# Kernel optimization log

Measured on AMD Instinct MI355X. Metric: run time of the kernel, lower is better.

## Reference

```python
import jax, jax.numpy as jnp
import numpy as np

EPS = 1e-5

def _bn(x, g, b):
    # training-mode batchnorm over all axes except the last (channel)
    axes = tuple(range(x.ndim - 1))
    m = x.mean(axis=axes, keepdims=True)
    v = x.var(axis=axes, keepdims=True)
    return (x - m) * jax.lax.rsqrt(v + EPS) * g + b

def setup_inputs() -> dict:
    key = jax.random.key(0)
    ks = jax.random.split(key, 9)
    B, N = 4, 4096
    def w(i, shape, fan_in):
        return jax.random.normal(ks[i], shape, jnp.float32) * np.float32(1.0 / np.sqrt(fan_in))
    return {
        "x": jax.random.normal(ks[0], (B, 3, N), jnp.float32),
        "Wq": w(1, (64, 3), 3),
        "Wkv": w(2, (128, 3), 3),
        "Wp1": w(3, (64, 3), 3),
        "Wp2": w(4, (64, 64), 64),
        "Wa": w(5, (64, 64), 64),
        "Wc1": w(6, (64, 64), 64),
        "Wsk": w(7, (64, 6), 6),
        "Wga": w(8, (64, 128), 128),
        "g_p": jnp.ones(64, jnp.float32), "b_p": jnp.zeros(64, jnp.float32),
        "g_a": jnp.ones(64, jnp.float32), "b_a": jnp.zeros(64, jnp.float32),
        "g_c": jnp.ones(64, jnp.float32), "b_c": jnp.zeros(64, jnp.float32),
        "g_sk": jnp.ones(64, jnp.float32), "b_sk": jnp.zeros(64, jnp.float32),
        "g_ga": jnp.ones(64, jnp.float32), "b_ga": jnp.zeros(64, jnp.float32),
        "k": 32,
    }

def reference(x, Wq, Wkv, Wp1, Wp2, Wa, Wc1, Wsk, Wga,
              g_p, b_p, g_a, b_a, g_c, b_c, g_sk, b_sk, g_ga, b_ga, k):
    # x: [B, 3, N] point cloud
    xt = jnp.transpose(x, (0, 2, 1))                      # [B, N, 3]
    B = xt.shape[0]
    # --- KNN neighbor grouping (irregular gather) ---
    sq = jnp.sum(xt * xt, axis=-1)                        # [B, N]
    dist = sq[:, :, None] + sq[:, None, :] - 2.0 * jnp.einsum('bnc,bmc->bnm', xt, xt)
    _, idx = jax.lax.top_k(-dist, k)                      # [B, N, k]
    grouped = xt[jnp.arange(B)[:, None, None], idx]       # [B, N, k, 3]
    rel = grouped - xt[:, :, None, :]                     # relative coords
    # --- local self-attention (1x1 conv QKV + position encoding) ---
    q = jnp.einsum('bnc,dc->bnd', xt, Wq)[:, :, None, :]  # [B, N, 1, 64]
    kv = jnp.einsum('bnkc,dc->bnkd', rel, Wkv)            # [B, N, k, 128]
    kf, vf = kv[..., :64], kv[..., 64:]
    pos = jnp.einsum('bnkd,ed->bnke',
                     jax.nn.relu(_bn(jnp.einsum('bnkc,dc->bnkd', rel, Wp1), g_p, b_p)),
                     Wp2)                                 # [B, N, k, 64]
    logits = jax.nn.relu(_bn(jnp.einsum('bnkd,ed->bnke', q - kf + pos, Wa), g_a, b_a))
    attn = jax.nn.softmax(logits, axis=2)                 # softmax over k neighbors
    agg = jnp.sum(attn * (vf + pos), axis=2)              # [B, N, 64]
    # --- pointnet conv-BN head + skip + fusion ---
    h = jax.nn.relu(_bn(jnp.einsum('bnd,ed->bne', agg, Wc1), g_c, b_c))
    nb_max = jnp.max(grouped, axis=2)                     # [B, N, 3] max-pool over neighbors
    sk = jax.nn.relu(_bn(jnp.einsum('bnc,dc->bnd',
                                    jnp.concatenate([xt, nb_max], axis=-1), Wsk), g_sk, b_sk))
    out = jax.nn.relu(_bn(jnp.einsum('bnc,dc->bnd',
                                     jnp.concatenate([h, sk], axis=-1), Wga), g_ga, b_ga))
    return jnp.transpose(out, (0, 2, 1))                  # [B, 64, N]
```

## Files before the change

### kernel.cpp

```cpp
#include <hip/hip_runtime.h>

#define NBATCH 4
#define NPTS   4096
#define NP     (NBATCH*NPTS)
#define KK     32
#define INF    __builtin_inff()

static const size_t OFF_PTS  = 0;
static const size_t OFF_IDX  = 65536;
static const size_t OFF_TSK  = 589824;
static const size_t OFF_TC   = 1638400;
static const size_t OFF_TGA  = 2686976;
static const size_t OFF_PREL = 3735552;
static const size_t OFF_PSK  = 3735568;
static const size_t OFF_PTA  = 3735696;
static const size_t OFF_PTC  = 3735824;
static const size_t OFF_PTGA = 3735952;
static const size_t OFF_AFF  = 3736080;

typedef __bf16 bf16x8  __attribute__((ext_vector_type(8)));
typedef float  floatx16 __attribute__((ext_vector_type(16)));
#define MFMA32(a,b,c) __builtin_amdgcn_mfma_f32_32x32x16_bf16(a, b, c, 0, 0, 0)

union F8 { bf16x8 v; unsigned short us[8]; uint4 q4; };

__device__ __forceinline__ unsigned short bfbits(float f) {
  unsigned u = __float_as_uint(f);
  return (unsigned short)((u + 0x7FFFu + ((u >> 16) & 1u)) >> 16);
}
__device__ __forceinline__ floatx16 zero16() {
  floatx16 v;
#pragma unroll
  for (int i = 0; i < 16; ++i) v[i] = 0.f;
  return v;
}
__device__ __forceinline__ float wsum(float v) {
#pragma unroll
  for (int o = 32; o; o >>= 1) v += __shfl_xor(v, o, 64);
  return v;
}
__device__ __forceinline__ int isum(int v) {
#pragma unroll
  for (int o = 32; o; o >>= 1) v += __shfl_xor(v, o);
  return v;
}

__global__ __launch_bounds__(256,1) void k_prep(const float* __restrict__ x, float4* __restrict__ pts,
                                                float* __restrict__ pta, float* __restrict__ ptc,
                                                float* __restrict__ ptga, float* __restrict__ prel9,
                                                float* __restrict__ psk128) {
  if (blockIdx.x == 0) {
    if (threadIdx.x < 128) {
      pta[threadIdx.x] = 0.f; ptc[threadIdx.x] = 0.f; ptga[threadIdx.x] = 0.f;
      psk128[threadIdx.x] = 0.f;
    }
    if (threadIdx.x < 16) prel9[threadIdx.x] = 0.f;
  }
  int g = blockIdx.x * 256 + threadIdx.x;
  int b = g / NPTS, n = g % NPTS;
  float vx = x[(b*3+0)*NPTS + n];
  float vy = x[(b*3+1)*NPTS + n];
  float vz = x[(b*3+2)*NPTS + n];
  pts[g] = make_float4(vx, vy, vz, vx*vx + vy*vy + vz*vz);
}

__global__ __launch_bounds__(256) void k_knn(const float4* __restrict__ pts, int* __restrict__ idx,
                                             const float* __restrict__ Wsk, float* __restrict__ tsk,
                                             float* __restrict__ prel9, float* __restrict__ psk128) {
  __shared__ __align__(16) float4 tile[1024];
  __shared__ int ocnt[4];
  __shared__ int lsel[128];
  __shared__ float rsum[9], psum[64], pss[64];
  const int tid  = threadIdx.x;
  const int w    = tid >> 6;
  const int lane = tid & 63;
  if (tid < 9)  rsum[tid] = 0.f;
  if (tid < 64) { psum[tid] = 0.f; pss[tid] = 0.f; }
  __syncthreads();
  const int n = blockIdx.x * 4 + w;
  const int batch = n >> 12;
  const float4* base = pts + batch * NPTS;
  const float4 me = pts[n];
  const float wk0 = Wsk[lane*6+0], wk1 = Wsk[lane*6+1], wk2 = Wsk[lane*6+2],
              wk3 = Wsk[lane*6+3], wk4 = Wsk[lane*6+4], wk5 = Wsk[lane*6+5];

  unsigned keys[64];
  unsigned t0 = 0xFFFFFFFFu, t1 = 0xFFFFFFFFu, t2 = 0xFFFFFFFFu, t3 = 0xFFFFFFFFu;
  for (int st = 0; st < 4; ++st) {
    __syncthreads();
#pragma unroll
    for (int r = 0; r < 4; ++r)
      tile[r*256 + tid] = base[st*1024 + r*256 + tid];
    __syncthreads();
#pragma unroll
    for (int j = 0; j < 16; ++j) {
      float4 p = tile[j*64 + lane];
      float dot = fmaf(me.x, p.x, fmaf(me.y, p.y, me.z * p.z));
      float d = fmaxf(fmaf(-2.f, dot, me.w + p.w), 0.f);
      unsigned k = __float_as_uint(d);
      keys[st*16 + j] = k;
      unsigned m = k, x;
      x = min(t0, m); m = max(t0, m); t0 = x;
      x = min(t1, m); m = max(t1, m); t1 = x;
      x = min(t2, m); m = max(t2, m); t2 = x;
      t3 = min(t3, m);
    }
  }

  unsigned glo = t0, ghi = t3;
#pragma unroll
  for (int o = 32; o; o >>= 1) {
    glo = min(glo, (unsigned)__shfl_xor((int)glo, o));
    ghi = max(ghi, (unsigned)__shfl_xor((int)ghi, o));
  }

  unsigned lo = glo, hi = ghi, tau = ghi;
  bool exact = false;
  while (lo < hi) {
    unsigned mid = lo + ((hi - lo) >> 1);
    int c = (t0 <= mid) + (t1 <= mid) + (t2 <= mid) + (t3 <= mid);
    c = isum(c);
    if (c == 32) { tau = mid; exact = true; break; }
    if (c > 32) hi = mid; else lo = mid + 1;
  }
  if (!exact) tau = lo;

  if (__ballot(t3 <= tau) != 0ull) {
    lo = glo; hi = tau; exact = false;
    while (lo < hi) {
      unsigned mid = lo + ((hi - lo) >> 1);
      int c = 0;
#pragma unroll
      for (int t = 0; t < 64; ++t) c += (keys[t] <= mid) ? 1 : 0;
      c = isum(c);
      if (c == 32) { tau = mid; exact = true; break; }
      if (c > 32) hi = mid; else lo = mid + 1;
    }
    if (!exact) tau = lo;
  }

  if (lane == 0) ocnt[w] = 0;
  int* op = idx + n * KK;
#pragma unroll
  for (int t = 0; t < 64; ++t) {
    bool take = exact ? (keys[t] <= tau) : (keys[t] < tau);
    if (take) {
      int s = atomicAdd(&ocnt[w], 1);
      int m = (t >> 4) * 1024 + (t & 15) * 64 + lane;
      op[s] = m; lsel[w*32 + s] = m;
    }
  }
  if (!exact) {
    unsigned long long em = 0;
#pragma unroll
    for (int t = 0; t < 64; ++t) if (keys[t] == tau) em |= 1ull << t;
    int n1 = ocnt[w];
    int need = 32 - n1;
    for (int f = 0; f < need; ++f) {
      int myt = em ? (int)__builtin_ctzll(em) : 64;
      int mym = (myt < 64) ? ((myt >> 4) * 1024 + (myt & 15) * 64 + lane) : 0x7FFFFFFF;
      int g = mym;
#pragma unroll
      for (int o = 32; o; o >>= 1) g = min(g, __shfl_xor(g, o));
      if (mym == g && myt < 64) { em &= em - 1; op[n1 + f] = mym; lsel[w*32 + n1 + f] = mym; }
    }
  }

  int mi = lsel[w*32 + (lane & 31)];
  float4 p = base[mi];
  bool act = lane < 32;
  float r0 = act ? p.x - me.x : 0.f;
  float r1 = act ? p.y - me.y : 0.f;
  float r2 = act ? p.z - me.z : 0.f;
  float vals[9] = { r0, r1, r2, r0*r0, r0*r1, r0*r2, r1*r1, r1*r2, r2*r2 };
#pragma unroll
  for (int t = 0; t < 9; ++t) {
    float rs = wsum(vals[t]);
    if (lane == 0) atomicAdd(&rsum[t], rs);
  }
  float nx = act ? p.x : -INF, ny = act ? p.y : -INF, nz = act ? p.z : -INF;
#pragma unroll
  for (int o = 32; o; o >>= 1) {
    nx = fmaxf(nx, __shfl_xor(nx, o));
    ny = fmaxf(ny, __shfl_xor(ny, o));
    nz = fmaxf(nz, __shfl_xor(nz, o));
  }
  float ts = fmaf(me.x, wk0, fmaf(me.y, wk1, fmaf(me.z, wk2,
             fmaf(nx, wk3, fmaf(ny, wk4, nz * wk5)))));
  tsk[n*64 + lane] = ts;
  atomicAdd(&psum[lane], ts);
  atomicAdd(&pss[lane], ts * ts);
  __syncthreads();
  if (tid < 9)  atomicAdd(&prel9[tid], rsum[tid]);
  if (tid < 64) atomicAdd(&psk128[tid], psum[tid]);
  else if (tid < 128) atomicAdd(&psk128[tid], pss[tid - 64]);
}

__global__ __launch_bounds__(64,1) void k_fin1(const float* __restrict__ prel9, const float* __restrict__ psk128,
                                               const float* __restrict__ Wp1,
                                               const float* __restrict__ g_p, const float* __restrict__ b_p,
                                               const float* __restrict__ g_sk, const float* __restrict__ b_sk,
                                               float* __restrict__ aff) {
  int d = threadIdx.x;
  double C = (double)NP * (double)KK;
  double mr0 = prel9[0]/C, mr1 = prel9[1]/C, mr2 = prel9[2]/C;
  double e00 = prel9[3]/C, e01 = prel9[4]/C, e02 = prel9[5]/C;
  double e11 = prel9[6]/C, e12 = prel9[7]/C, e22 = prel9[8]/C;
  double w0 = Wp1[d*3+0], w1 = Wp1[d*3+1], w2 = Wp1[d*3+2];
  double mu  = w0*mr0 + w1*mr1 + w2*mr2;
  double ex2 = w0*w0*e00 + w1*w1*e11 + w2*w2*e22 + 2.0*(w0*w1*e01 + w0*w2*e02 + w1*w2*e12);
  double var = ex2 - mu*mu;
  double sc  = (double)g_p[d] / sqrt(var + 1e-5);
  aff[0*64 + d] = (float)sc;
  aff[1*64 + d] = (float)((double)b_p[d] - mu*sc);
  double mean = (double)psk128[d] / (double)NP;
  double v2   = (double)psk128[64+d] / (double)NP - mean*mean;
  double sc4  = (double)g_sk[d] / sqrt(v2 + 1e-5);
  aff[6*64 + d] = (float)sc4;
  aff[7*64 + d] = (float)((double)b_sk[d] - mean*sc4);
}

__global__ __launch_bounds__(64,1) void k_fin2(const float* __restrict__ st, double C,
                                               const float* __restrict__ g, const float* __restrict__ b,
                                               float* __restrict__ s_out, float* __restrict__ o_out) {
  int d = threadIdx.x;
  double mean = (double)st[d] / C;
  double var  = (double)st[64 + d] / C - mean*mean;
  double sc   = (double)g[d] / sqrt(var + 1e-5);
  s_out[d] = (float)sc;
  o_out[d] = (float)((double)b[d] - mean*sc);
}

template<int MODE>
__global__ __launch_bounds__(256,1) void k_entry(const float4* __restrict__ pts, const int* __restrict__ idx,
                                                 const float* __restrict__ Wq, const float* __restrict__ Wkv,
                                                 const float* __restrict__ Wp1, const float* __restrict__ Wp2,
                                                 const float* __restrict__ Wa, const float* __restrict__ Wc1,
                                                 const float* __restrict__ aff, float* __restrict__ pstats,
                                                 float* __restrict__ tc) {
  __shared__ __align__(16) unsigned short ybuf[4][32][72];
  __shared__ __align__(16) float aggbuf[4][64];
  __shared__ float psum[64], pss[64];
  if (threadIdx.x < 64) { psum[threadIdx.x] = 0.f; pss[threadIdx.x] = 0.f; }
  __syncthreads();
  const int lane = threadIdx.x & 63;
  const int w    = threadIdx.x >> 6;
  const int c    = lane & 31;
  const int q5   = lane >> 5;

  F8 B0[2];
#pragma unroll
  for (int nt = 0; nt < 2; ++nt)
#pragma unroll
    for (int t = 0; t < 8; ++t)
      B0[nt].us[t] = (q5 == 0 && t < 3) ? bfbits(Wp1[(nt*32+c)*3 + t]) : (unsigned short)0;

  F8 Bs[4][2], B2[4][2];
#pragma unroll
  for (int kt = 0; kt < 4; ++kt)
#pragma unroll
    for (int h = 0; h < 2; ++h) {
      const float* p2 = Wp2 + (h*32+c)*64 + kt*16 + q5*8;
      float4 a = *(const float4*)p2, b = *(const float4*)(p2 + 4);
      Bs[kt][h].us[0]=bfbits(a.x); Bs[kt][h].us[1]=bfbits(a.y); Bs[kt][h].us[2]=bfbits(a.z); Bs[kt][h].us[3]=bfbits(a.w);
      Bs[kt][h].us[4]=bfbits(b.x); Bs[kt][h].us[5]=bfbits(b.y); Bs[kt][h].us[6]=bfbits(b.z); Bs[kt][h].us[7]=bfbits(b.w);
      const float* pa = Wa + (h*32+c)*64 + kt*16 + q5*8;
      float4 e = *(const float4*)pa, f = *(const float4*)(pa + 4);
      B2[kt][h].us[0]=bfbits(e.x); B2[kt][h].us[1]=bfbits(e.y); B2[kt][h].us[2]=bfbits(e.z); B2[kt][h].us[3]=bfbits(e.w);
      B2[kt][h].us[4]=bfbits(f.x); B2[kt][h].us[5]=bfbits(f.y); B2[kt][h].us[6]=bfbits(f.z); B2[kt][h].us[7]=bfbits(f.w);
    }

  F8 Bk4[4];
#pragma unroll
  for (int nt = 0; nt < 4; ++nt) {
    if (MODE == 0 && nt >= 2) { for (int t = 0; t < 8; ++t) Bk4[nt].us[t] = 0; continue; }
    int e = (nt & 1)*32 + c;
#pragma unroll
    for (int t = 0; t < 8; ++t)
      Bk4[nt].us[t] = (q5 == 0 && t < 3)
        ? bfbits(nt < 2 ? -Wkv[e*3 + t] : Wkv[(64+e)*3 + t]) : (unsigned short)0;
  }

  const float s1a = aff[c],      o1a = aff[64+c];
  const float s1b = aff[32+c],   o1b = aff[96+c];
  float s2a = 0.f, o2a = 0.f, s2b = 0.f, o2b = 0.f;
  if (MODE == 1) { s2a = aff[128+c]; o2a = aff[192+c]; s2b = aff[160+c]; o2b = aff[224+c]; }
  const float wqa0 = Wq[c*3+0],      wqa1 = Wq[c*3+1],      wqa2 = Wq[c*3+2];
  const float wqb0 = Wq[(32+c)*3+0], wqb1 = Wq[(32+c)*3+1], wqb2 = Wq[(32+c)*3+2];

  const int wave_id = blockIdx.x * 4 + w;
  const int n0 = wave_id * 8;
  const int batch = n0 >> 12;
  const float4* base = pts + batch * NPTS;

  float4 me = pts[n0];
  float4 pp = base[idx[n0*KK + c]];

  for (int pi = 0; pi < 8; ++pi) {
    const int n = n0 + pi;
    float4 men = me, ppn = pp;
    if (pi < 7) {
      men = pts[n + 1];
      ppn = base[idx[(n + 1)*KK + c]];
    }
    const float r0 = pp.x - me.x, r1 = pp.y - me.y, r2 = pp.z - me.z;
    F8 relA;
#pragma unroll
    for (int t = 0; t < 8; ++t) relA.us[t] = 0;
    if (q5 == 0) { relA.us[0] = bfbits(r0); relA.us[1] = bfbits(r1); relA.us[2] = bfbits(r2); }

    const floatx16 z = zero16();
    floatx16 y0 = MFMA32(relA.v, B0[0].v, z);
    floatx16 y1 = MFMA32(relA.v, B0[1].v, z);
#pragma unroll
    for (int r = 0; r < 16; ++r) {
      int row = (r & 3) + 8*(r >> 2) + 4*q5;
      ybuf[w][row][c]      = bfbits(fmaxf(fmaf(y0[r], s1a, o1a), 0.f));
      ybuf[w][row][32 + c] = bfbits(fmaxf(fmaf(y1[r], s1b, o1b), 0.f));
    }
    F8 Ay[4];
#pragma unroll
    for (int kt = 0; kt < 4; ++kt) Ay[kt].q4 = *(const uint4*)&ybuf[w][c][kt*16 + q5*8];

    floatx16 Cp0 = z, Cp1 = z;
#pragma unroll
    for (int kt = 0; kt < 4; ++kt) {
      Cp0 = MFMA32(Ay[kt].v, Bs[kt][0].v, Cp0);
      Cp1 = MFMA32(Ay[kt].v, Bs[kt][1].v, Cp1);
    }
    floatx16 Cu0 = MFMA32(relA.v, Bk4[0].v, Cp0);
    floatx16 Cu1 = MFMA32(relA.v, Bk4[1].v, Cp1);
    if (MODE == 1) {
      Cp0 = MFMA32(relA.v, Bk4[2].v, Cp0);
      Cp1 = MFMA32(relA.v, Bk4[3].v, Cp1);
    }
    const float qa = fmaf(me.x, wqa0, fmaf(me.y, wqa1, me.z * wqa2));
    const float qb = fmaf(me.x, wqb0, fmaf(me.y, wqb1, me.z * wqb2));
#pragma unroll
    for (int r = 0; r < 16; ++r) {
      int row = (r & 3) + 8*(r >> 2) + 4*q5;
      ybuf[w][row][c]      = bfbits(Cu0[r] + qa);
      ybuf[w][row][32 + c] = bfbits(Cu1[r] + qb);
    }
    F8 Au[4];
#pragma unroll
    for (int kt = 0; kt < 4; ++kt) Au[kt].q4 = *(const uint4*)&ybuf[w][c][kt*16 + q5*8];
    floatx16 Ct0 = z, Ct1 = z;
#pragma unroll
    for (int kt = 0; kt < 4; ++kt) {
      Ct0 = MFMA32(Au[kt].v, B2[kt][0].v, Ct0);
      Ct1 = MFMA32(Au[kt].v, B2[kt][1].v, Ct1);
    }

    if (MODE == 0) {
      float sa = 0.f, qqa = 0.f, sb = 0.f, qqb = 0.f;
#pragma unroll
      for (int r = 0; r < 16; ++r) {
        sa += Ct0[r]; qqa = fmaf(Ct0[r], Ct0[r], qqa);
        sb += Ct1[r]; qqb = fmaf(Ct1[r], Ct1[r], qqb);
      }
      sa += __shfl_xor(sa, 32); qqa += __shfl_xor(qqa, 32);
      sb += __shfl_xor(sb, 32); qqb += __shfl_xor(qqb, 32);
      if (q5 == 0) {
        atomicAdd(&psum[c], sa);      atomicAdd(&pss[c], qqa);
        atomicAdd(&psum[32+c], sb);   atomicAdd(&pss[32+c], qqb);
      }
    } else {
      float ma = -INF, mb = -INF;
#pragma unroll
      for (int r = 0; r < 16; ++r) {
        float la = fmaxf(fmaf(Ct0[r], s2a, o2a), 0.f); Ct0[r] = la; ma = fmaxf(ma, la);
        float lb = fmaxf(fmaf(Ct1[r], s2b, o2b), 0.f); Ct1[r] = lb; mb = fmaxf(mb, lb);
      }
      ma = fmaxf(ma, __shfl_xor(ma, 32));
      mb = fmaxf(mb, __shfl_xor(mb, 32));
      float sa = 0.f, sb = 0.f, aga = 0.f, agb = 0.f;
#pragma unroll
      for (int r = 0; r < 16; ++r) {
        float ta = __expf(Ct0[r] - ma); sa += ta; aga = fmaf(ta, Cp0[r], aga);
        float tb = __expf(Ct1[r] - mb); sb += tb; agb = fmaf(tb, Cp1[r], agb);
      }
      sa += __shfl_xor(sa, 32); aga += __shfl_xor(aga, 32);
      sb += __shfl_xor(sb, 32); agb += __shfl_xor(agb, 32);
      if (q5 == 0) {
        aggbuf[w][c]      = aga / sa;
        aggbuf[w][32 + c] = agb / sb;
      }
      float acc = 0.f;
#pragma unroll
      for (int g = 0; g < 16; ++g) {
        float4 av = *(const float4*)&aggbuf[w][g*4];
        const float4 wv = *(const float4*)(Wc1 + lane*64 + g*4);
        acc = fmaf(av.x, wv.x, fmaf(av.y, wv.y, fmaf(av.z, wv.z, fmaf(av.w, wv.w, acc))));
      }
      tc[n*64 + lane] = acc;
      atomicAdd(&psum[lane], acc);
      atomicAdd(&pss[lane], acc * acc);
    }
    me = men; pp = ppn;
  }
  __syncthreads();
  if (threadIdx.x < 64) atomicAdd(&pstats[threadIdx.x], psum[threadIdx.x]);
  else if (threadIdx.x < 128) atomicAdd(&pstats[threadIdx.x], pss[threadIdx.x - 64]);
}

__global__ __launch_bounds__(256,1) void k_final(const float* __restrict__ tcb, const float* __restrict__ tskb,
                                                 const float* __restrict__ Wga, const float* __restrict__ aff,
                                                 float* __restrict__ tga, float* __restrict__ pstats) {
  __shared__ __align__(16) float hb[4][64];
  __shared__ __align__(16) float sb[4][64];
  __shared__ float psum[64], pss[64];
  if (threadIdx.x < 64) { psum[threadIdx.x] = 0.f; pss[threadIdx.x] = 0.f; }
  __syncthreads();
  const int lane = threadIdx.x & 63;
  const int w    = threadIdx.x >> 6;
  const int n = blockIdx.x * 4 + w;
  hb[w][lane] = fmaxf(fmaf(tcb[n*64 + lane],  aff[256 + lane], aff[320 + lane]), 0.f);
  sb[w][lane] = fmaxf(fmaf(tskb[n*64 + lane], aff[384 + lane], aff[448 + lane]), 0.f);
  float g0=0,g1=0,g2=0,g3=0;
#pragma unroll
  for (int d = 0; d < 64; d += 4) {
    const float4 hv = *(const float4*)&hb[w][d];
    const float4 wg = *(const float4*)(Wga + lane*128 + d);
    g0 = fmaf(hv.x, wg.x, g0);
    g1 = fmaf(hv.y, wg.y, g1);
    g2 = fmaf(hv.z, wg.z, g2);
    g3 = fmaf(hv.w, wg.w, g3);
  }
#pragma unroll
  for (int d = 0; d < 64; d += 4) {
    const float4 sv = *(const float4*)&sb[w][d];
    const float4 wg = *(const float4*)(Wga + lane*128 + 64 + d);
    g0 = fmaf(sv.x, wg.x, g0);
    g1 = fmaf(sv.y, wg.y, g1);
    g2 = fmaf(sv.z, wg.z, g2);
    g3 = fmaf(sv.w, wg.w, g3);
  }
  const float tg = (g0+g1) + (g2+g3);
  tga[n*64 + lane] = tg;
  atomicAdd(&psum[lane], tg);
  atomicAdd(&pss[lane], tg * tg);
  __syncthreads();
  if (threadIdx.x < 64) atomicAdd(&pstats[threadIdx.x], psum[threadIdx.x]);
  else if (threadIdx.x < 128) atomicAdd(&pstats[threadIdx.x], pss[threadIdx.x - 64]);
}

__global__ __launch_bounds__(256,1) void k_out(const float* __restrict__ tga, const float* __restrict__ aff,
                                               float* __restrict__ out) {
  int g = blockIdx.x * 256 + threadIdx.x;
  int nn = g & 4095;
  int e  = (g >> 12) & 63;
  int b  = g >> 18;
  float v = tga[((b << 12) + nn) * 64 + e];
  out[g] = fmaxf(fmaf(v, aff[512 + e], aff[576 + e]), 0.f);
}

extern "C" void kernel_launch(void* const* d_in, const int* in_sizes, int n_in,
                              void* d_out, int out_size, void* d_ws, size_t ws_size,
                              hipStream_t stream) {
  const float* x    = (const float*)d_in[0];
  const float* Wq   = (const float*)d_in[1];
  const float* Wkv  = (const float*)d_in[2];
  const float* Wp1  = (const float*)d_in[3];
  const float* Wp2  = (const float*)d_in[4];
  const float* Wa   = (const float*)d_in[5];
  const float* Wc1  = (const float*)d_in[6];
  const float* Wsk  = (const float*)d_in[7];
  const float* Wga  = (const float*)d_in[8];
  const float* g_p  = (const float*)d_in[9];
  const float* b_p  = (const float*)d_in[10];
  const float* g_a  = (const float*)d_in[11];
  const float* b_a  = (const float*)d_in[12];
  const float* g_c  = (const float*)d_in[13];
  const float* b_c  = (const float*)d_in[14];
  const float* g_sk = (const float*)d_in[15];
  const float* b_sk = (const float*)d_in[16];
  const float* g_ga = (const float*)d_in[17];
  const float* b_ga = (const float*)d_in[18];
  float* W = (float*)d_ws;
  float4*  pts   = (float4*)(W + OFF_PTS);
  int*     idx   = (int*)(W + OFF_IDX);
  float*   tsk   = W + OFF_TSK;
  float*   tc    = W + OFF_TC;
  float*   tga   = W + OFF_TGA;
  float*   prel9 = W + OFF_PREL;
  float*   psk   = W + OFF_PSK;
  float*   pta   = W + OFF_PTA;
  float*   ptc   = W + OFF_PTC;
  float*   ptga  = W + OFF_PTGA;
  float*   aff   = W + OFF_AFF;
  float*   out   = (float*)d_out;

  k_prep<<<64, 256, 0, stream>>>(x, pts, pta, ptc, ptga, prel9, psk);
  k_knn<<<4096, 256, 0, stream>>>(pts, idx, Wsk, tsk, prel9, psk);
  k_fin1<<<1, 64, 0, stream>>>(prel9, psk, Wp1, g_p, b_p, g_sk, b_sk, aff);
  k_entry<0><<<512, 256, 0, stream>>>(pts, idx, Wq, Wkv, Wp1, Wp2, Wa, nullptr, aff, pta, nullptr);
  k_fin2<<<1, 64, 0, stream>>>(pta, (double)NP * (double)KK, g_a, b_a, aff + 128, aff + 192);
  k_entry<1><<<512, 256, 0, stream>>>(pts, idx, Wq, Wkv, Wp1, Wp2, Wa, Wc1, aff, ptc, tc);
  k_fin2<<<1, 64, 0, stream>>>(ptc, (double)NP, g_c, b_c, aff + 256, aff + 320);
  k_final<<<4096, 256, 0, stream>>>(tc, tsk, Wga, aff, tga, ptga);
  k_fin2<<<1, 64, 0, stream>>>(ptga, (double)NP, g_ga, b_ga, aff + 512, aff + 576);
  k_out<<<4096, 256, 0, stream>>>(tga, aff, out);
}
```

Baseline: 470.5 us.

## Keep per-lane top-5 key/index registers instead of 64-key array in KNN

Replaces the per-lane array of 64 distance keys with a register-resident sorted top-5 list of keys and indices, so the common selection path works only on those 5 candidates. When some lane has more than 5 of the k nearest, a fallback recomputes distances from global memory during the refined binary search and the final selection. The aim is to cut register pressure (64 VGPRs of keys) to raise occupancy and reduce selection work. The cost is extra insertion ops per point and a slow recompute path for clustered lanes.

```diff
diff --git a/kernel.cpp b/kernel.cpp
--- a/kernel.cpp
+++ b/kernel.cpp
@@ -84,8 +84,11 @@
   const float wk0 = Wsk[lane*6+0], wk1 = Wsk[lane*6+1], wk2 = Wsk[lane*6+2],
               wk3 = Wsk[lane*6+3], wk4 = Wsk[lane*6+4], wk5 = Wsk[lane*6+5];
 
-  unsigned keys[64];
-  unsigned t0 = 0xFFFFFFFFu, t1 = 0xFFFFFFFFu, t2 = 0xFFFFFFFFu, t3 = 0xFFFFFFFFu;
+  unsigned ka0 = 0xFFFFFFFFu, ka1 = 0xFFFFFFFFu, ka2 = 0xFFFFFFFFu,
+           ka3 = 0xFFFFFFFFu, ka4 = 0xFFFFFFFFu;
+  int ia0 = 0, ia1 = 0, ia2 = 0, ia3 = 0, ia4 = 0;
+#define PINS(KR, IR) { bool cc = key < KR; unsigned tk = cc ? KR : key; int ti = cc ? IR : id; \
+                       KR = cc ? key : KR; IR = cc ? id : IR; key = tk; id = ti; }
   for (int st = 0; st < 4; ++st) {
     __syncthreads();
 #pragma unroll
@@ -97,17 +100,14 @@
       float4 p = tile[j*64 + lane];
       float dot = fmaf(me.x, p.x, fmaf(me.y, p.y, me.z * p.z));
       float d = fmaxf(fmaf(-2.f, dot, me.w + p.w), 0.f);
-      unsigned k = __float_as_uint(d);
-      keys[st*16 + j] = k;
-      unsigned m = k, x;
-      x = min(t0, m); m = max(t0, m); t0 = x;
-      x = min(t1, m); m = max(t1, m); t1 = x;
-      x = min(t2, m); m = max(t2, m); t2 = x;
-      t3 = min(t3, m);
-    }
-  }
-
-  unsigned glo = t0, ghi = t3;
+      unsigned key = __float_as_uint(d);
+      int id = st*1024 + j*64 + lane;
+      PINS(ka0, ia0) PINS(ka1, ia1) PINS(ka2, ia2) PINS(ka3, ia3) PINS(ka4, ia4)
+    }
+  }
+#undef PINS
+
+  unsigned glo = ka0, ghi = ka4;
 #pragma unroll
   for (int o = 32; o; o >>= 1) {
     glo = min(glo, (unsigned)__shfl_xor((int)glo, o));
@@ -118,51 +118,83 @@
   bool exact = false;
   while (lo < hi) {
     unsigned mid = lo + ((hi - lo) >> 1);
-    int c = (t0 <= mid) + (t1 <= mid) + (t2 <= mid) + (t3 <= mid);
+    int c = (ka0 <= mid) + (ka1 <= mid) + (ka2 <= mid) + (ka3 <= mid) + (ka4 <= mid);
     c = isum(c);
     if (c == 32) { tau = mid; exact = true; break; }
     if (c > 32) hi = mid; else lo = mid + 1;
   }
   if (!exact) tau = lo;
 
-  if (__ballot(t3 <= tau) != 0ull) {
+  if (lane == 0) ocnt[w] = 0;
+  int* op = idx + n * KK;
+
+  if (__ballot(ka4 <= tau) == 0ull) {
+    unsigned kk[5] = { ka0, ka1, ka2, ka3, ka4 };
+    int      ii[5] = { ia0, ia1, ia2, ia3, ia4 };
+#pragma unroll
+    for (int r = 0; r < 5; ++r) {
+      bool take = exact ? (kk[r] <= tau) : (kk[r] < tau);
+      if (take) {
+        int s = atomicAdd(&ocnt[w], 1);
+        op[s] = ii[r]; lsel[w*32 + s] = ii[r];
+      }
+    }
+    if (!exact) {
+      unsigned used = 0;
+      int n1 = ocnt[w];
+      int need = KK - n1;
+      for (int f = 0; f < need; ++f) {
+        int my = 0x7FFFFFFF, which = -1;
+#pragma unroll
+        for (int r = 0; r < 5; ++r)
+          if (!((used >> r) & 1) && kk[r] == tau && ii[r] < my) { my = ii[r]; which = r; }
+        int g = my;
+#pragma unroll
+        for (int o = 32; o; o >>= 1) g = min(g, __shfl_xor(g, o));
+        if (my == g && which >= 0) { used |= 1u << which; op[n1 + f] = my; lsel[w*32 + n1 + f] = my; }
+      }
+    }
+  } else {
     lo = glo; hi = tau; exact = false;
     while (lo < hi) {
       unsigned mid = lo + ((hi - lo) >> 1);
       int c = 0;
-#pragma unroll
-      for (int t = 0; t < 64; ++t) c += (keys[t] <= mid) ? 1 : 0;
+      for (int j = 0; j < 64; ++j) {
+        float4 p = base[j*64 + lane];
+        float dot = fmaf(me.x, p.x, fmaf(me.y, p.y, me.z * p.z));
+        float d = fmaxf(fmaf(-2.f, dot, me.w + p.w), 0.f);
+        c += (__float_as_uint(d) <= mid) ? 1 : 0;
+      }
       c = isum(c);
       if (c == 32) { tau = mid; exact = true; break; }
       if (c > 32) hi = mid; else lo = mid + 1;
     }
     if (!exact) tau = lo;
-  }
-
-  if (lane == 0) ocnt[w] = 0;
-  int* op = idx + n * KK;
-#pragma unroll
-  for (int t = 0; t < 64; ++t) {
-    bool take = exact ? (keys[t] <= tau) : (keys[t] < tau);
-    if (take) {
-      int s = atomicAdd(&ocnt[w], 1);
-      int m = (t >> 4) * 1024 + (t & 15) * 64 + lane;
-      op[s] = m; lsel[w*32 + s] = m;
-    }
-  }
-  if (!exact) {
     unsigned long long em = 0;
-#pragma unroll
-    for (int t = 0; t < 64; ++t) if (keys[t] == tau) em |= 1ull << t;
-    int n1 = ocnt[w];
-    int need = 32 - n1;
-    for (int f = 0; f < need; ++f) {
-      int myt = em ? (int)__builtin_ctzll(em) : 64;
-      int mym = (myt < 64) ? ((myt >> 4) * 1024 + (myt & 15) * 64 + lane) : 0x7FFFFFFF;
-      int g = mym;
-#pragma unroll
-      for (int o = 32; o; o >>= 1) g = min(g, __shfl_xor(g, o));
-      if (mym == g && myt < 64) { em &= em - 1; op[n1 + f] = mym; lsel[w*32 + n1 + f] = mym; }
+    for (int j = 0; j < 64; ++j) {
+      float4 p = base[j*64 + lane];
+      float dot = fmaf(me.x, p.x, fmaf(me.y, p.y, me.z * p.z));
+      float d = fmaxf(fmaf(-2.f, dot, me.w + p.w), 0.f);
+      unsigned key = __float_as_uint(d);
+      bool take = exact ? (key <= tau) : (key < tau);
+      if (take) {
+        int s = atomicAdd(&ocnt[w], 1);
+        int m = j*64 + lane;
+        if (s < KK) { op[s] = m; lsel[w*32 + s] = m; }
+      }
+      if (key == tau) em |= 1ull << j;
+    }
+    if (!exact) {
+      int n1 = ocnt[w];
+      int need = KK - n1;
+      for (int f = 0; f < need; ++f) {
+        int myj = em ? (int)__builtin_ctzll(em) : 64;
+        int mym = (myj < 64) ? (myj*64 + lane) : 0x7FFFFFFF;
+        int g = mym;
+#pragma unroll
+        for (int o = 32; o; o >>= 1) g = min(g, __shfl_xor(g, o));
+        if (mym == g && myj < 64) { em &= em - 1; op[n1 + f] = mym; lsel[w*32 + n1 + f] = mym; }
+      }
     }
   }
 
```

Result: slower. 562.7 us (+19.6%).
